# Optimization experiments

Measured on AMD Instinct MI355X. Metric: run time of the kernel, lower is better.

Reference implementation:

```python
import jax, jax.numpy as jnp
import numpy as np

V, E, H2, TAG = 32000, 128, 256, 9
H = H2 // 2          # per-direction LSTM hidden
B, T = 128, 512


def setup_inputs() -> dict:
    key = jax.random.key(0)
    ks = jax.random.split(key, 15)
    s = 0.08
    n = lambda k, shp: jax.random.normal(k, shp, dtype=jnp.float32) * s
    return {
        "sentence": jax.random.randint(ks[0], (B, T), 0, V, dtype=jnp.int32),
        "tags": jax.random.randint(ks[1], (B, T), 0, TAG, dtype=jnp.int32),
        "mask": jnp.ones((B, T), dtype=bool),
        "embedding": n(ks[2], (V, E)),
        "w_ih_f": n(ks[3], (4 * H, E)),
        "w_hh_f": n(ks[4], (4 * H, H)),
        "b_f": n(ks[5], (4 * H,)),
        "w_ih_b": n(ks[6], (4 * H, E)),
        "w_hh_b": n(ks[7], (4 * H, H)),
        "b_b": n(ks[8], (4 * H,)),
        "w_out": n(ks[9], (TAG, H2)),
        "b_out": n(ks[10], (TAG,)),
        "start_trans": n(ks[11], (TAG,)),
        "end_trans": n(ks[12], (TAG,)),
        "trans": n(ks[13], (TAG, TAG)),
    }


def _lstm_dir(xp, w_hh):
    """xp: [T,B,4H] precomputed input projections (incl. bias). Returns h seq [T,B,H]."""
    Hn = w_hh.shape[1]
    Bn = xp.shape[1]

    def step(carry, x_t):
        h, c = carry
        g = x_t + h @ w_hh.T                       # [B,4H]
        i, f, gg, o = jnp.split(g, 4, axis=-1)     # torch gate order: i,f,g,o
        c = jax.nn.sigmoid(f) * c + jax.nn.sigmoid(i) * jnp.tanh(gg)
        h = jax.nn.sigmoid(o) * jnp.tanh(c)
        return (h, c), h

    init = (jnp.zeros((Bn, Hn), xp.dtype), jnp.zeros((Bn, Hn), xp.dtype))
    _, hs = jax.lax.scan(step, init, xp)
    return hs


def reference(sentence, tags, mask, embedding, w_ih_f, w_hh_f, b_f,
              w_ih_b, w_hh_b, b_b, w_out, b_out, start_trans, end_trans, trans):
    # ---- BiLSTM emissions ----
    x = embedding[sentence]                 # [B,T,E]
    xt = jnp.swapaxes(x, 0, 1)              # [T,B,E]
    h_f = _lstm_dir(xt @ w_ih_f.T + b_f, w_hh_f)                 # [T,B,H]
    h_b = _lstm_dir((xt @ w_ih_b.T + b_b)[::-1], w_hh_b)[::-1]   # [T,B,H]
    hcat = jnp.concatenate([h_f, h_b], axis=-1)                  # [T,B,2H]
    emissions = hcat @ w_out.T + b_out                           # [T,B,TAG]

    m = mask.T.astype(emissions.dtype)      # [T,B]
    tt = tags.T                             # [T,B]
    bidx = jnp.arange(tt.shape[1])

    # ---- CRF numerator (score of gold path), torchcrf semantics ----
    num0 = start_trans[tt[0]] + emissions[0, bidx, tt[0]]        # [B]

    def num_step(score, inp):
        e_t, t_prev, t_cur, m_t = inp
        return score + (trans[t_prev, t_cur] + e_t[bidx, t_cur]) * m_t, None

    num, _ = jax.lax.scan(num_step, num0, (emissions[1:], tt[:-1], tt[1:], m[1:]))
    seq_ends = mask.sum(axis=1).astype(jnp.int32) - 1            # [B]
    last_tags = tt[seq_ends, bidx]
    num = num + end_trans[last_tags]

    # ---- CRF log-partition (forward algorithm) ----
    alpha0 = start_trans + emissions[0]                          # [B,TAG]

    def fwd_step(alpha, inp):
        e_t, m_t = inp
        nxt = jax.nn.logsumexp(alpha[:, :, None] + trans[None] + e_t[:, None, :], axis=1)
        return jnp.where(m_t[:, None] > 0, nxt, alpha), None

    alpha, _ = jax.lax.scan(fwd_step, alpha0, (emissions[1:], m[1:]))
    logZ = jax.nn.logsumexp(alpha + end_trans, axis=1)           # [B]

    # forward returns -crf(...) with reduction='mean' => mean negative log-likelihood
    return -jnp.mean(num - logZ)
```

## Files before the change

kernel.cpp:

```cpp
#include <hip/hip_runtime.h>
#include <hip/hip_bf16.h>
#include <cstdint>
#include <cstddef>

#define NB   128
#define NT   512
#define NE   128
#define NH   128
#define NG   512
#define NTAG 9

typedef __bf16 bf16;
typedef __bf16 bf16x4 __attribute__((ext_vector_type(4)));
typedef __bf16 bf16x8 __attribute__((ext_vector_type(8)));
typedef _Float16 f16;
typedef _Float16 f16x2 __attribute__((ext_vector_type(2)));
typedef _Float16 f16x8 __attribute__((ext_vector_type(8)));
typedef float  floatx4 __attribute__((ext_vector_type(4)));

__device__ __forceinline__ float bflo_f32(unsigned u) {
  union { unsigned x; float f; } c; c.x = u << 16; return c.f;
}
__device__ __forceinline__ float bfhi_f32(unsigned u) {
  union { unsigned x; float f; } c; c.x = u & 0xFFFF0000u; return c.f;
}
__device__ __forceinline__ f16x2 pkh(float a, float b) {
  return __builtin_bit_cast(f16x2, __builtin_amdgcn_cvt_pkrtz(a, b));
}
__device__ __forceinline__ void block_sync_lds() {
  asm volatile("s_waitcnt lgkmcnt(0)\n\ts_barrier" ::: "memory");
}

__device__ __forceinline__ f16x2 sigm_h(f16x2 x) {
  const f16x2 lo = {(f16)(-2.5f), (f16)(-2.5f)}, hi = {(f16)2.5f, (f16)2.5f};
  x = __builtin_elementwise_min(__builtin_elementwise_max(x, lo), hi);
  f16x2 t = x * x;
  f16x2 p = t * (f16)0.0010154f + (f16)(-0.019144f);
  p = t * p + (f16)0.24964f;
  return x * p + (f16)0.5f;
}
__device__ __forceinline__ f16x2 tanh_h(f16x2 x) {
  const f16x2 lo = {(f16)(-1.5f), (f16)(-1.5f)}, hi = {(f16)1.5f, (f16)1.5f};
  x = __builtin_elementwise_min(__builtin_elementwise_max(x, lo), hi);
  f16x2 t = x * x;
  f16x2 p = t * (f16)0.045172f + (f16)(-0.27334f);
  p = t * p + (f16)0.98976f;
  return x * p;
}

__global__ __launch_bounds__(256, 1) void k_prep(
    const float* __restrict__ emb, const float* __restrict__ w_ih_f,
    const float* __restrict__ w_ih_b, const int* __restrict__ sentence,
    bf16* __restrict__ embb, bf16* __restrict__ wihf, bf16* __restrict__ wihb,
    int* __restrict__ sentT)
{
  const int gid = blockIdx.x * 256 + threadIdx.x;
  const int gsz = gridDim.x * 256;
  for (int i = gid; i < 512000; i += gsz) {
    const float* s = emb + (size_t)i * 8;
    bf16x8 v;
    #pragma unroll
    for (int j = 0; j < 8; ++j) v[j] = (bf16)s[j];
    *(bf16x8*)&embb[(size_t)i * 8] = v;
  }
  for (int i = gid; i < 8192; i += gsz) {
    const float* s = w_ih_f + (size_t)i * 8;
    bf16x8 v;
    #pragma unroll
    for (int j = 0; j < 8; ++j) v[j] = (bf16)s[j];
    *(bf16x8*)&wihf[(size_t)i * 8] = v;
  }
  for (int i = gid; i < 8192; i += gsz) {
    const float* s = w_ih_b + (size_t)i * 8;
    bf16x8 v;
    #pragma unroll
    for (int j = 0; j < 8; ++j) v[j] = (bf16)s[j];
    *(bf16x8*)&wihb[(size_t)i * 8] = v;
  }
  for (int i = gid; i < NT * NB; i += gsz) {
    const int t = i >> 7, b = i & 127;
    sentT[i] = sentence[b * NT + t];
  }
}

__global__ __launch_bounds__(256, 1) void k_embed_proj(
    const int* __restrict__ sentT, const bf16* __restrict__ embb,
    const bf16* __restrict__ wihf, const bf16* __restrict__ wihb,
    const float* __restrict__ b_f, const float* __restrict__ b_b,
    bf16* __restrict__ xp_f, bf16* __restrict__ xp_b)
{
  __shared__ bf16 Cld[128 * 136];
  const int mb = blockIdx.x, nb = blockIdx.y;
  const int colbase = nb * 128;
  const int tid = threadIdx.x;
  const int wv = tid >> 6, lane = tid & 63;
  const int lrow = lane & 15, quad = lane >> 4;
  const int m0 = (wv & 1) * 64, n0 = (wv >> 1) * 64;

  int tokv[4];
  #pragma unroll
  for (int mt = 0; mt < 4; ++mt)
    tokv[mt] = sentT[mb * NB + m0 + mt * 16 + lrow];
  bf16x8 af[4][4];
  #pragma unroll
  for (int kk = 0; kk < 4; ++kk)
    #pragma unroll
    for (int mt = 0; mt < 4; ++mt)
      af[kk][mt] = *(const bf16x8*)&embb[(size_t)tokv[mt] * NE + kk * 32 + quad * 8];

  #pragma unroll
  for (int d = 0; d < 2; ++d) {
    const bf16* W     = (d == 0) ? (wihf + (size_t)nb * 128 * 128)
                                 : (wihb + (size_t)nb * 128 * 128);
    const float* bias = (d == 0) ? (b_f + colbase) : (b_b + colbase);
    bf16* outdir      = (d == 0) ? xp_f : xp_b;

    floatx4 acc[4][4] = {};
    #pragma unroll
    for (int kk = 0; kk < 4; ++kk) {
      bf16x8 bfr[4];
      #pragma unroll
      for (int nt = 0; nt < 4; ++nt)
        bfr[nt] = *(const bf16x8*)&W[(size_t)(n0 + nt * 16 + lrow) * 128 + kk * 32 + quad * 8];
      #pragma unroll
      for (int mt = 0; mt < 4; ++mt)
        #pragma unroll
        for (int nt = 0; nt < 4; ++nt)
          acc[mt][nt] = __builtin_amdgcn_mfma_f32_16x16x32_bf16(af[kk][mt], bfr[nt], acc[mt][nt], 0, 0, 0);
    }
    float bv[4];
    #pragma unroll
    for (int nt = 0; nt < 4; ++nt) bv[nt] = bias[n0 + nt * 16 + lrow];
    if (d == 1) __syncthreads();
    #pragma unroll
    for (int mt = 0; mt < 4; ++mt)
      #pragma unroll
      for (int nt = 0; nt < 4; ++nt) {
        bf16x4 v4;
        #pragma unroll
        for (int rr = 0; rr < 4; ++rr) v4[rr] = (bf16)(acc[mt][nt][rr] + bv[nt]);
        *(bf16x4*)&Cld[(n0 + nt * 16 + lrow) * 136 + m0 + mt * 16 + quad * 4] = v4;
      }
    __syncthreads();
    bf16* outbase = outdir + ((size_t)mb * 8) * (512 * 16) + (size_t)colbase * 16;
    #pragma unroll
    for (int it = 0; it < 8; ++it) {
      const int p = it * 256 + tid;
      const int bb = p >> 8, n = (p >> 1) & 127, half = p & 1;
      *(bf16x8*)(outbase + ((size_t)bb * 512 + n) * 16 + half * 8) =
          *(const bf16x8*)&Cld[n * 136 + bb * 16 + half * 8];
    }
  }
}

#define LSTM_STEP(PX, RB, WB)                                                  \
  do {                                                                         \
    f16x8 af[4];                                                               \
    _Pragma("unroll")                                                          \
    for (int kk = 0; kk < 4; ++kk)                                             \
      af[kk] = *(const f16x8*)&(RB)[lane * 8 + kk * 512];                      \
    floatx4 acc[4];                                                            \
    _Pragma("unroll")                                                          \
    for (int g = 0; g < 4; ++g) {                                              \
      acc[g][0] = bflo_f32(PX[g][0]); acc[g][1] = bfhi_f32(PX[g][0]);          \
      acc[g][2] = bflo_f32(PX[g][1]); acc[g][3] = bfhi_f32(PX[g][1]);          \
    }                                                                          \
    _Pragma("unroll")                                                          \
    for (int g = 0; g < 4; ++g) {             \
      uint2 u = *(const uint2*)pg[g];                                          \
      PX[g][0] = u.x; PX[g][1] = u.y;                                          \
      pg[g] += dstep_x;                                                        \
    }                                                                          \
    _Pragma("unroll")                                                          \
    for (int kk = 0; kk < 4; ++kk)                                             \
      _Pragma("unroll")                                                        \
      for (int g = 0; g < 4; ++g)                                              \
        acc[g] = __builtin_amdgcn_mfma_f32_16x16x32_f16(af[kk], wf[g][kk],     \
                                                        acc[g], 0, 0, 0);      \
    {                                                                          \
      f16x2 iv, fv, gv, ov, h2;                                                \
      iv = sigm_h(pkh(acc[0][0], acc[0][1]));                                  \
      fv = sigm_h(pkh(acc[1][0], acc[1][1]));                                  \
      gv = tanh_h(pkh(acc[2][0], acc[2][1]));                                  \
      ov = sigm_h(pkh(acc[3][0], acc[3][1]));                                  \
      c01 = fv * c01 + iv * gv;                                                \
      h2 = ov * tanh_h(c01);                                                   \
      (WB)[wboff + 0 * 8] = h2[0]; (WB)[wboff + 1 * 8] = h2[1];                \
      hop[0 * NH] = h2[0]; hop[1 * NH] = h2[1];                                \
      iv = sigm_h(pkh(acc[0][2], acc[0][3]));                                  \
      fv = sigm_h(pkh(acc[1][2], acc[1][3]));                                  \
      gv = tanh_h(pkh(acc[2][2], acc[2][3]));                                  \
      ov = sigm_h(pkh(acc[3][2], acc[3][3]));                                  \
      c23 = fv * c23 + iv * gv;                                                \
      h2 = ov * tanh_h(c23);                                                   \
      (WB)[wboff + 2 * 8] = h2[0]; (WB)[wboff + 3 * 8] = h2[1];                \
      hop[2 * NH] = h2[0]; hop[3 * NH] = h2[1];                                \
    }                                                                          \
    hop += dstep_h;                                                            \
    block_sync_lds();                                                          \
  } while (0)

__global__ __launch_bounds__(512, 1) void k_lstm(
    const bf16* __restrict__ xp_f, const bf16* __restrict__ xp_b,
    const float* __restrict__ w_hh_f, const float* __restrict__ w_hh_b,
    f16* __restrict__ h_f, f16* __restrict__ h_b)
{
  __shared__ f16 hfrag[2][2048];
  const int wg = blockIdx.x;
  const int dir = wg >> 3;
  const int bb = wg & 7;
  const int b0 = bb * 16;
  const bf16* __restrict__ xp   = dir ? xp_b   : xp_f;
  const float* __restrict__ Whh = dir ? w_hh_b : w_hh_f;
  f16* __restrict__ hout        = dir ? h_b    : h_f;
  const int tid = threadIdx.x;
  const int wv = tid >> 6, lane = tid & 63;
  const int lrow = lane & 15, quad = lane >> 4;
  const int hc = wv * 16 + lrow;

  f16x8 wf[4][4];
  #pragma unroll
  for (int g = 0; g < 4; ++g)
    #pragma unroll
    for (int kk = 0; kk < 4; ++kk) {
      const float* src = Whh + (size_t)(g * 128 + hc) * 128 + kk * 32 + quad * 8;
      f16x8 v;
      #pragma unroll
      for (int j = 0; j < 8; ++j) v[j] = (f16)src[j];
      wf[g][kk] = v;
    }
  {
    f16x2 z = {(f16)0.f, (f16)0.f};
    *(f16x2*)&hfrag[0][tid * 2] = z;
    *(f16x2*)&hfrag[0][1024 + tid * 2] = z;
  }

  const int t0 = dir ? (NT - 1) : 0;
  const ptrdiff_t dstep_x = dir ? -(ptrdiff_t)(8 * 512 * 16) : (ptrdiff_t)(8 * 512 * 16);
  const ptrdiff_t dstep_h = dir ? -(ptrdiff_t)(NB * NH) : (ptrdiff_t)(NB * NH);

  const bf16* pg[4];
  unsigned pxA[4][2], pxB[4][2];
  #pragma unroll
  for (int g = 0; g < 4; ++g)
    pg[g] = xp + (((size_t)t0 * 8 + bb) * 512 + g * 128 + hc) * 16 + quad * 4;
  #pragma unroll
  for (int g = 0; g < 4; ++g) {
    uint2 u = *(const uint2*)pg[g];
    pxA[g][0] = u.x; pxA[g][1] = u.y;
    pg[g] += dstep_x;
  }
  #pragma unroll
  for (int g = 0; g < 4; ++g) {
    uint2 u = *(const uint2*)pg[g];
    pxB[g][0] = u.x; pxB[g][1] = u.y;
    pg[g] += dstep_x;
  }
  f16* hop = hout + ((size_t)t0 * NB + b0 + quad * 4) * NH + hc;
  const int wboff = ((hc >> 3) * 16 + quad * 4) * 8 + (hc & 7);
  f16x2 c01 = {(f16)0.f, (f16)0.f}, c23 = {(f16)0.f, (f16)0.f};
  block_sync_lds();

  for (int s = 0; s < NT; s += 2) {
    LSTM_STEP(pxA, hfrag[0], hfrag[1]);
    LSTM_STEP(pxB, hfrag[1], hfrag[0]);
  }
}

__global__ __launch_bounds__(256, 1) void k_emis(
    const f16* __restrict__ h_f, const f16* __restrict__ h_b,
    const float* __restrict__ w_out, const float* __restrict__ b_out,
    float* __restrict__ emis)
{
  const int tid = threadIdx.x;
  const int wv = tid >> 6, lane = tid & 63;
  const int lrow = lane & 15, quad = lane >> 4;
  const int m0 = blockIdx.x * 64 + wv * 16;
  const size_t mrow = (size_t)(m0 + lrow);

  f16x8 wo[8];
  #pragma unroll
  for (int kk = 0; kk < 8; ++kk) {
    f16x8 v;
    #pragma unroll
    for (int j = 0; j < 8; ++j) v[j] = (f16)0.0f;
    if (lrow < NTAG) {
      const float* src = w_out + (size_t)lrow * 256 + kk * 32 + quad * 8;
      #pragma unroll
      for (int j = 0; j < 8; ++j) v[j] = (f16)src[j];
    }
    wo[kk] = v;
  }
  floatx4 acc = {};
  #pragma unroll
  for (int kk = 0; kk < 4; ++kk) {
    const f16x8 a = *(const f16x8*)&h_f[mrow * NH + kk * 32 + quad * 8];
    acc = __builtin_amdgcn_mfma_f32_16x16x32_f16(a, wo[kk], acc, 0, 0, 0);
  }
  #pragma unroll
  for (int kk = 0; kk < 4; ++kk) {
    const f16x8 a = *(const f16x8*)&h_b[mrow * NH + kk * 32 + quad * 8];
    acc = __builtin_amdgcn_mfma_f32_16x16x32_f16(a, wo[kk + 4], acc, 0, 0, 0);
  }
  if (lrow < NTAG) {
    const float bb = b_out[lrow];
    #pragma unroll
    for (int rr = 0; rr < 4; ++rr)
      emis[(size_t)(m0 + quad * 4 + rr) * NTAG + lrow] = acc[rr] + bb;
  }
}

__global__ __launch_bounds__(192, 1) void k_crfA(
    const float* __restrict__ emis, const float* __restrict__ trans,
    float* __restrict__ P)
{
  const int tid = threadIdx.x;
  const int grp = tid >> 4;
  const int j = tid & 15;
  const int c = blockIdx.x;
  const int b = blockIdx.y;
  const int gbase = (tid & 63) & ~15;
  const int i = (grp < 9) ? grp : 8;
  const int jj = (j < NTAG) ? j : 0;

  float tcol[NTAG];
  #pragma unroll
  for (int k = 0; k < NTAG; ++k) tcol[k] = trans[k * NTAG + jj];

  const int t1 = 1 + 8 * c;
  const int nst = (c == 63) ? 6 : 7;
  int eo = (t1 * NB + b) * NTAG + jj;
  float alpha = (j < NTAG) ? (trans[i * NTAG + jj] + emis[eo]) : -1e30f;
  for (int tt = 0; tt < nst; ++tt) {
    eo += NB * NTAG;
    const float e = emis[eo];
    float a[NTAG];
    #pragma unroll
    for (int k = 0; k < NTAG; ++k) a[k] = __shfl(alpha, gbase + k, 64) + tcol[k];
    float m = a[0];
    #pragma unroll
    for (int k = 1; k < NTAG; ++k) m = fmaxf(m, a[k]);
    float ssum = 0.0f;
    #pragma unroll
    for (int k = 0; k < NTAG; ++k) ssum += __expf(a[k] - m);
    alpha = m + __logf(ssum) + e;
  }
  if (grp < NTAG && j < NTAG)
    P[(((size_t)b * 64 + c) * NTAG + j) * NTAG + i] = alpha;
}

#define CHUNK_STEP(PC)                                                         \
  do {                                                                         \
    float a[NTAG];                                                             \
    _Pragma("unroll")                                                          \
    for (int k = 0; k < NTAG; ++k) a[k] = __shfl(alpha, gbase + k, 64) + PC[k];\
    float m = a[0];                                                            \
    _Pragma("unroll")                                                          \
    for (int k = 1; k < NTAG; ++k) m = fmaxf(m, a[k]);                         \
    float ssum = 0.0f;                                                         \
    _Pragma("unroll")                                                          \
    for (int k = 0; k < NTAG; ++k) ssum += __expf(a[k] - m);                   \
    alpha = m + __logf(ssum);                                                  \
  } while (0)

__global__ __launch_bounds__(256, 1) void k_crfB(
    const float* __restrict__ emis, const int* __restrict__ tags,
    const float* __restrict__ start_trans, const float* __restrict__ end_trans,
    const float* __restrict__ trans, const float* __restrict__ P,
    float* __restrict__ res)
{
  const int tid = threadIdx.x;
  const int grp = tid >> 4;
  const int j = tid & 15;
  const int b = blockIdx.x * 16 + grp;
  const int gbase = (tid & 63) & ~15;
  const int jj = (j < NTAG) ? j : 0;

  float nsum = 0.0f;
  for (int t = 1 + j; t < NT; t += 16) {
    const int tp = tags[b * NT + t - 1];
    const int tc = tags[b * NT + t];
    nsum += trans[tp * NTAG + tc] + emis[(t * NB + b) * NTAG + tc];
  }
  if (j == 0) {
    const int tg0 = tags[b * NT];
    const int tgl = tags[b * NT + NT - 1];
    nsum += start_trans[tg0] + emis[b * NTAG + tg0] + end_trans[tgl];
  }
  #pragma unroll
  for (int m = 8; m >= 1; m >>= 1) nsum += __shfl_xor(nsum, m, 16);

  float alpha = (j < NTAG) ? (start_trans[j] + emis[b * NTAG + jj]) : -1e30f;
  const float* Pb = P + ((size_t)b * 64 * 81) + jj * NTAG;
  float pA[NTAG], pB[NTAG];
  #pragma unroll
  for (int k = 0; k < NTAG; ++k) pA[k] = Pb[k];
  #pragma unroll
  for (int k = 0; k < NTAG; ++k) pB[k] = Pb[81 + k];
  for (int c = 0; c < 64; c += 2) {
    CHUNK_STEP(pA);
    if (c + 2 < 64) {
      #pragma unroll
      for (int k = 0; k < NTAG; ++k) pA[k] = Pb[(c + 2) * 81 + k];
    }
    CHUNK_STEP(pB);
    if (c + 3 < 64) {
      #pragma unroll
      for (int k = 0; k < NTAG; ++k) pB[k] = Pb[(c + 3) * 81 + k];
    }
  }
  const float av = (j < NTAG) ? (alpha + end_trans[j]) : -1e30f;
  float vals[NTAG];
  #pragma unroll
  for (int k = 0; k < NTAG; ++k) vals[k] = __shfl(av, gbase + k, 64);
  float m2 = vals[0];
  #pragma unroll
  for (int k = 1; k < NTAG; ++k) m2 = fmaxf(m2, vals[k]);
  float s2 = 0.0f;
  #pragma unroll
  for (int k = 0; k < NTAG; ++k) s2 += __expf(vals[k] - m2);
  const float logZ = m2 + __logf(s2);
  if (j == 0) res[b] = logZ - nsum;
}

__global__ __launch_bounds__(128, 1) void k_mean(const float* __restrict__ res,
                                                 float* __restrict__ out)
{
  const int tid = threadIdx.x;
  float v = res[tid];
  #pragma unroll
  for (int m = 32; m >= 1; m >>= 1) v += __shfl_xor(v, m, 64);
  __shared__ float sv[2];
  if ((tid & 63) == 0) sv[tid >> 6] = v;
  __syncthreads();
  if (tid == 0) out[0] = (sv[0] + sv[1]) * (1.0f / 128.0f);
}

extern "C" void kernel_launch(void* const* d_in, const int* in_sizes, int n_in,
                              void* d_out, int out_size, void* d_ws, size_t ws_size,
                              hipStream_t stream)
{
  (void)in_sizes; (void)n_in; (void)out_size; (void)ws_size;
  const int*   sentence    = (const int*)d_in[0];
  const int*   tags        = (const int*)d_in[1];
  const float* embedding   = (const float*)d_in[3];
  const float* w_ih_f      = (const float*)d_in[4];
  const float* w_hh_f      = (const float*)d_in[5];
  const float* b_f         = (const float*)d_in[6];
  const float* w_ih_b      = (const float*)d_in[7];
  const float* w_hh_b      = (const float*)d_in[8];
  const float* b_b         = (const float*)d_in[9];
  const float* w_out       = (const float*)d_in[10];
  const float* b_out       = (const float*)d_in[11];
  const float* start_trans = (const float*)d_in[12];
  const float* end_trans   = (const float*)d_in[13];
  const float* trans       = (const float*)d_in[14];
  float* out = (float*)d_out;

  char* ws = (char*)d_ws;
  bf16*  xp_f = (bf16*)(ws);
  bf16*  xp_b = (bf16*)(ws + 67108864);
  f16*   h_f  = (f16*)(ws + 134217728);
  f16*   h_b  = (f16*)(ws + 150994944);
  float* emis = (float*)(ws + 167772160);
  bf16*  embb  = (bf16*)(ws + 134217728);
  bf16*  wihf  = (bf16*)(ws + 142606336);
  bf16*  wihb  = (bf16*)(ws + 142737408);
  int*   sentT = (int*) (ws + 142868480);
  float* P     = (float*)(ws + 134217728);
  float* res   = (float*)(ws + 136871936);

  k_prep<<<256, 256, 0, stream>>>(embedding, w_ih_f, w_ih_b, sentence,
                                  embb, wihf, wihb, sentT);
  k_embed_proj<<<dim3(512, 4), 256, 0, stream>>>(sentT, embb, wihf, wihb,
                                                 b_f, b_b, xp_f, xp_b);
  k_lstm<<<16, 512, 0, stream>>>(xp_f, xp_b, w_hh_f, w_hh_b, h_f, h_b);
  k_emis<<<1024, 256, 0, stream>>>(h_f, h_b, w_out, b_out, emis);
  k_crfA<<<dim3(64, 128), 192, 0, stream>>>(emis, trans, P);
  k_crfB<<<8, 256, 0, stream>>>(emis, tags, start_trans, end_trans, trans, P, res);
  k_mean<<<1, 128, 0, stream>>>(res, out);
}
```

Before: 581.3 us.

## Halve LSTM workgroup to 4 waves, each handling two hidden-column slices

The recurrent LSTM kernel now runs 256 threads per block instead of 512, with each wave computing two 16-column hidden slices (cs=0,1) and holding twice the recurrent weight fragments in registers. This reduces the number of waves participating in the per-step block barrier and gives each wave more independent MFMA work to interleave. In exchange it doubles per-thread register use for weights and accumulators, which risks spills, and halves the available wave-level parallelism per step.

```diff
diff --git a/kernel.cpp b/kernel.cpp
--- a/kernel.cpp
+++ b/kernel.cpp
@@ -159,48 +159,60 @@
     _Pragma("unroll")                                                          \
     for (int kk = 0; kk < 4; ++kk)                                             \
       af[kk] = *(const f16x8*)&(RB)[lane * 8 + kk * 512];                      \
-    floatx4 acc[4];                                                            \
-    _Pragma("unroll")                                                          \
-    for (int g = 0; g < 4; ++g) {                                              \
-      acc[g][0] = bflo_f32(PX[g][0]); acc[g][1] = bfhi_f32(PX[g][0]);          \
-      acc[g][2] = bflo_f32(PX[g][1]); acc[g][3] = bfhi_f32(PX[g][1]);          \
-    }                                                                          \
-    _Pragma("unroll")                                                          \
-    for (int g = 0; g < 4; ++g) {             \
-      uint2 u = *(const uint2*)pg[g];                                          \
-      PX[g][0] = u.x; PX[g][1] = u.y;                                          \
-      pg[g] += dstep_x;                                                        \
-    }                                                                          \
+    floatx4 acc[2][4];                                                         \
+    _Pragma("unroll")                                                          \
+    for (int cs = 0; cs < 2; ++cs)                                             \
+      _Pragma("unroll")                                                        \
+      for (int g = 0; g < 4; ++g) {                                            \
+        acc[cs][g][0] = bflo_f32(PX[cs][g][0]);                                \
+        acc[cs][g][1] = bfhi_f32(PX[cs][g][0]);                                \
+        acc[cs][g][2] = bflo_f32(PX[cs][g][1]);                                \
+        acc[cs][g][3] = bfhi_f32(PX[cs][g][1]);                                \
+      }                                                                        \
+    _Pragma("unroll")                                                          \
+    for (int cs = 0; cs < 2; ++cs)            \
+      _Pragma("unroll")                                                        \
+      for (int g = 0; g < 4; ++g) {                                            \
+        uint2 u = *(const uint2*)(pg[g] + cs * 1024);                          \
+        PX[cs][g][0] = u.x; PX[cs][g][1] = u.y;                                \
+      }                                                                        \
+    _Pragma("unroll")                                                          \
+    for (int g = 0; g < 4; ++g) pg[g] += dstep_x;                              \
     _Pragma("unroll")                                                          \
     for (int kk = 0; kk < 4; ++kk)                                             \
       _Pragma("unroll")                                                        \
-      for (int g = 0; g < 4; ++g)                                              \
-        acc[g] = __builtin_amdgcn_mfma_f32_16x16x32_f16(af[kk], wf[g][kk],     \
-                                                        acc[g], 0, 0, 0);      \
-    {                                                                          \
+      for (int cs = 0; cs < 2; ++cs)                                           \
+        _Pragma("unroll")                                                      \
+        for (int g = 0; g < 4; ++g)                                            \
+          acc[cs][g] = __builtin_amdgcn_mfma_f32_16x16x32_f16(                 \
+              af[kk], wf[cs][g][kk], acc[cs][g], 0, 0, 0);                     \
+    _Pragma("unroll")                                                          \
+    for (int cs = 0; cs < 2; ++cs) {                                           \
       f16x2 iv, fv, gv, ov, h2;                                                \
-      iv = sigm_h(pkh(acc[0][0], acc[0][1]));                                  \
-      fv = sigm_h(pkh(acc[1][0], acc[1][1]));                                  \
-      gv = tanh_h(pkh(acc[2][0], acc[2][1]));                                  \
-      ov = sigm_h(pkh(acc[3][0], acc[3][1]));                                  \
-      c01 = fv * c01 + iv * gv;                                                \
-      h2 = ov * tanh_h(c01);                                                   \
-      (WB)[wboff + 0 * 8] = h2[0]; (WB)[wboff + 1 * 8] = h2[1];                \
-      hop[0 * NH] = h2[0]; hop[1 * NH] = h2[1];                                \
-      iv = sigm_h(pkh(acc[0][2], acc[0][3]));                                  \
-      fv = sigm_h(pkh(acc[1][2], acc[1][3]));                                  \
-      gv = tanh_h(pkh(acc[2][2], acc[2][3]));                                  \
-      ov = sigm_h(pkh(acc[3][2], acc[3][3]));                                  \
-      c23 = fv * c23 + iv * gv;                                                \
-      h2 = ov * tanh_h(c23);                                                   \
-      (WB)[wboff + 2 * 8] = h2[0]; (WB)[wboff + 3 * 8] = h2[1];                \
-      hop[2 * NH] = h2[0]; hop[3 * NH] = h2[1];                                \
+      iv = sigm_h(pkh(acc[cs][0][0], acc[cs][0][1]));                          \
+      fv = sigm_h(pkh(acc[cs][1][0], acc[cs][1][1]));                          \
+      gv = tanh_h(pkh(acc[cs][2][0], acc[cs][2][1]));                          \
+      ov = sigm_h(pkh(acc[cs][3][0], acc[cs][3][1]));                          \
+      c01[cs] = fv * c01[cs] + iv * gv;                                        \
+      h2 = ov * tanh_h(c01[cs]);                                               \
+      (WB)[wboff + cs * 1024 + 0 * 8] = h2[0];                                 \
+      (WB)[wboff + cs * 1024 + 1 * 8] = h2[1];                                 \
+      hop[cs * 64 + 0 * NH] = h2[0]; hop[cs * 64 + 1 * NH] = h2[1];            \
+      iv = sigm_h(pkh(acc[cs][0][2], acc[cs][0][3]));                          \
+      fv = sigm_h(pkh(acc[cs][1][2], acc[cs][1][3]));                          \
+      gv = tanh_h(pkh(acc[cs][2][2], acc[cs][2][3]));                          \
+      ov = sigm_h(pkh(acc[cs][3][2], acc[cs][3][3]));                          \
+      c23[cs] = fv * c23[cs] + iv * gv;                                        \
+      h2 = ov * tanh_h(c23[cs]);                                               \
+      (WB)[wboff + cs * 1024 + 2 * 8] = h2[0];                                 \
+      (WB)[wboff + cs * 1024 + 3 * 8] = h2[1];                                 \
+      hop[cs * 64 + 2 * NH] = h2[0]; hop[cs * 64 + 3 * NH] = h2[1];            \
     }                                                                          \
     hop += dstep_h;                                                            \
     block_sync_lds();                                                          \
   } while (0)
 
-__global__ __launch_bounds__(512, 1) void k_lstm(
+__global__ __launch_bounds__(256, 1) void k_lstm(
     const bf16* __restrict__ xp_f, const bf16* __restrict__ xp_b,
     const float* __restrict__ w_hh_f, const float* __restrict__ w_hh_b,
     f16* __restrict__ h_f, f16* __restrict__ h_b)
@@ -218,21 +230,24 @@
   const int lrow = lane & 15, quad = lane >> 4;
   const int hc = wv * 16 + lrow;
 
-  f16x8 wf[4][4];
-  #pragma unroll
-  for (int g = 0; g < 4; ++g)
-    #pragma unroll
-    for (int kk = 0; kk < 4; ++kk) {
-      const float* src = Whh + (size_t)(g * 128 + hc) * 128 + kk * 32 + quad * 8;
-      f16x8 v;
-      #pragma unroll
-      for (int j = 0; j < 8; ++j) v[j] = (f16)src[j];
-      wf[g][kk] = v;
-    }
+  f16x8 wf[2][4][4];
+  #pragma unroll
+  for (int cs = 0; cs < 2; ++cs)
+    #pragma unroll
+    for (int g = 0; g < 4; ++g)
+      #pragma unroll
+      for (int kk = 0; kk < 4; ++kk) {
+        const float* src = Whh + (size_t)(g * 128 + cs * 64 + hc) * 128 + kk * 32 + quad * 8;
+        f16x8 v;
+        #pragma unroll
+        for (int j = 0; j < 8; ++j) v[j] = (f16)src[j];
+        wf[cs][g][kk] = v;
+      }
   {
-    f16x2 z = {(f16)0.f, (f16)0.f};
-    *(f16x2*)&hfrag[0][tid * 2] = z;
-    *(f16x2*)&hfrag[0][1024 + tid * 2] = z;
+    f16x8 z;
+    #pragma unroll
+    for (int j = 0; j < 8; ++j) z[j] = (f16)0.f;
+    *(f16x8*)&hfrag[0][tid * 8] = z;
   }
 
   const int t0 = dir ? (NT - 1) : 0;
@@ -240,25 +255,37 @@
   const ptrdiff_t dstep_h = dir ? -(ptrdiff_t)(NB * NH) : (ptrdiff_t)(NB * NH);
 
   const bf16* pg[4];
-  unsigned pxA[4][2], pxB[4][2];
+  unsigned pxA[2][4][2], pxB[2][4][2];
   #pragma unroll
   for (int g = 0; g < 4; ++g)
     pg[g] = xp + (((size_t)t0 * 8 + bb) * 512 + g * 128 + hc) * 16 + quad * 4;
   #pragma unroll
-  for (int g = 0; g < 4; ++g) {
-    uint2 u = *(const uint2*)pg[g];
-    pxA[g][0] = u.x; pxA[g][1] = u.y;
-    pg[g] += dstep_x;
-  }
-  #pragma unroll
-  for (int g = 0; g < 4; ++g) {
-    uint2 u = *(const uint2*)pg[g];
-    pxB[g][0] = u.x; pxB[g][1] = u.y;
-    pg[g] += dstep_x;
-  }
+  for (int cs = 0; cs < 2; ++cs)
+    #pragma unroll
+    for (int g = 0; g < 4; ++g) {
+      uint2 u = *(const uint2*)(pg[g] + cs * 1024);
+      pxA[cs][g][0] = u.x; pxA[cs][g][1] = u.y;
+    }
+  #pragma unroll
+  for (int g = 0; g < 4; ++g) pg[g] += dstep_x;
+  #pragma unroll
+  for (int cs = 0; cs < 2; ++cs)
+    #pragma unroll
+    for (int g = 0; g < 4; ++g) {
+      uint2 u = *(const uint2*)(pg[g] + cs * 1024);
+      pxB[cs][g][0] = u.x; pxB[cs][g][1] = u.y;
+    }
+  #pragma unroll
+  for (int g = 0; g < 4; ++g) pg[g] += dstep_x;
+
   f16* hop = hout + ((size_t)t0 * NB + b0 + quad * 4) * NH + hc;
   const int wboff = ((hc >> 3) * 16 + quad * 4) * 8 + (hc & 7);
-  f16x2 c01 = {(f16)0.f, (f16)0.f}, c23 = {(f16)0.f, (f16)0.f};
+  f16x2 c01[2], c23[2];
+  #pragma unroll
+  for (int cs = 0; cs < 2; ++cs) {
+    c01[cs][0] = (f16)0.f; c01[cs][1] = (f16)0.f;
+    c23[cs][0] = (f16)0.f; c23[cs][1] = (f16)0.f;
+  }
   block_sync_lds();
 
   for (int s = 0; s < NT; s += 2) {
@@ -474,7 +501,7 @@
                                   embb, wihf, wihb, sentT);
   k_embed_proj<<<dim3(512, 4), 256, 0, stream>>>(sentT, embb, wihf, wihb,
                                                  b_f, b_b, xp_f, xp_b);
-  k_lstm<<<16, 512, 0, stream>>>(xp_f, xp_b, w_hh_f, w_hh_b, h_f, h_b);
+  k_lstm<<<16, 256, 0, stream>>>(xp_f, xp_b, w_hh_f, w_hh_b, h_f, h_b);
   k_emis<<<1024, 256, 0, stream>>>(h_f, h_b, w_out, b_out, emis);
   k_crfA<<<dim3(64, 128), 192, 0, stream>>>(emis, trans, P);
   k_crfB<<<8, 256, 0, stream>>>(emis, tags, start_trans, end_trans, trans, P, res);
```

Result: slower. 746.3 us (+28.4%).

## Fuse CRF combine and mean reduction into chunk kernel via atomic counters

Applied to the files above, without the earlier changes.

The CRF chunk kernel now counts finished chunks per batch element with an atomic counter. The last block for each batch element then runs the gold-path score and the chunk-combine log-partition, and a global counter lets the final block compute the mean. The counters are zeroed in the emission kernel. This removes two kernel launches and their gaps, at the cost of atomics, fences and a serialized tail in a few blocks.

```diff
diff --git a/kernel.cpp b/kernel.cpp
--- a/kernel.cpp
+++ b/kernel.cpp
@@ -270,9 +270,13 @@
 __global__ __launch_bounds__(256, 1) void k_emis(
     const f16* __restrict__ h_f, const f16* __restrict__ h_b,
     const float* __restrict__ w_out, const float* __restrict__ b_out,
-    float* __restrict__ emis)
+    float* __restrict__ emis, int* __restrict__ cnt_b, int* __restrict__ cnt_all)
 {
   const int tid = threadIdx.x;
+  if (blockIdx.x == 0) {
+    if (tid < 128) cnt_b[tid] = 0;
+    if (tid == 128) *cnt_all = 0;
+  }
   const int wv = tid >> 6, lane = tid & 63;
   const int lrow = lane & 15, quad = lane >> 4;
   const int m0 = blockIdx.x * 64 + wv * 16;
@@ -310,10 +314,29 @@
   }
 }
 
+#define CHUNK_STEP(PC)                                                         \
+  do {                                                                         \
+    float a[NTAG];                                                             \
+    _Pragma("unroll")                                                          \
+    for (int k = 0; k < NTAG; ++k) a[k] = __shfl(alpha, gbase + k, 64) + PC[k];\
+    float m = a[0];                                                            \
+    _Pragma("unroll")                                                          \
+    for (int k = 1; k < NTAG; ++k) m = fmaxf(m, a[k]);                         \
+    float ssum = 0.0f;                                                         \
+    _Pragma("unroll")                                                          \
+    for (int k = 0; k < NTAG; ++k) ssum += __expf(a[k] - m);                   \
+    alpha = m + __logf(ssum);                                                  \
+  } while (0)
+
 __global__ __launch_bounds__(192, 1) void k_crfA(
     const float* __restrict__ emis, const float* __restrict__ trans,
-    float* __restrict__ P)
-{
+    const int* __restrict__ tags, const float* __restrict__ start_trans,
+    const float* __restrict__ end_trans, float* __restrict__ P,
+    int* __restrict__ cnt_b, int* __restrict__ cnt_all,
+    float* __restrict__ res, float* __restrict__ out)
+{
+  __shared__ int s_last;
+  __shared__ float sv[2];
   const int tid = threadIdx.x;
   const int grp = tid >> 4;
   const int j = tid & 15;
@@ -323,115 +346,108 @@
   const int i = (grp < 9) ? grp : 8;
   const int jj = (j < NTAG) ? j : 0;
 
-  float tcol[NTAG];
-  #pragma unroll
-  for (int k = 0; k < NTAG; ++k) tcol[k] = trans[k * NTAG + jj];
-
-  const int t1 = 1 + 8 * c;
-  const int nst = (c == 63) ? 6 : 7;
-  int eo = (t1 * NB + b) * NTAG + jj;
-  float alpha = (j < NTAG) ? (trans[i * NTAG + jj] + emis[eo]) : -1e30f;
-  for (int tt = 0; tt < nst; ++tt) {
-    eo += NB * NTAG;
-    const float e = emis[eo];
-    float a[NTAG];
-    #pragma unroll
-    for (int k = 0; k < NTAG; ++k) a[k] = __shfl(alpha, gbase + k, 64) + tcol[k];
-    float m = a[0];
-    #pragma unroll
-    for (int k = 1; k < NTAG; ++k) m = fmaxf(m, a[k]);
-    float ssum = 0.0f;
-    #pragma unroll
-    for (int k = 0; k < NTAG; ++k) ssum += __expf(a[k] - m);
-    alpha = m + __logf(ssum) + e;
-  }
-  if (grp < NTAG && j < NTAG)
-    P[(((size_t)b * 64 + c) * NTAG + j) * NTAG + i] = alpha;
-}
-
-#define CHUNK_STEP(PC)                                                         \
-  do {                                                                         \
-    float a[NTAG];                                                             \
-    _Pragma("unroll")                                                          \
-    for (int k = 0; k < NTAG; ++k) a[k] = __shfl(alpha, gbase + k, 64) + PC[k];\
-    float m = a[0];                                                            \
-    _Pragma("unroll")                                                          \
-    for (int k = 1; k < NTAG; ++k) m = fmaxf(m, a[k]);                         \
-    float ssum = 0.0f;                                                         \
-    _Pragma("unroll")                                                          \
-    for (int k = 0; k < NTAG; ++k) ssum += __expf(a[k] - m);                   \
-    alpha = m + __logf(ssum);                                                  \
-  } while (0)
-
-__global__ __launch_bounds__(256, 1) void k_crfB(
-    const float* __restrict__ emis, const int* __restrict__ tags,
-    const float* __restrict__ start_trans, const float* __restrict__ end_trans,
-    const float* __restrict__ trans, const float* __restrict__ P,
-    float* __restrict__ res)
-{
-  const int tid = threadIdx.x;
-  const int grp = tid >> 4;
-  const int j = tid & 15;
-  const int b = blockIdx.x * 16 + grp;
-  const int gbase = (tid & 63) & ~15;
-  const int jj = (j < NTAG) ? j : 0;
-
-  float nsum = 0.0f;
-  for (int t = 1 + j; t < NT; t += 16) {
-    const int tp = tags[b * NT + t - 1];
-    const int tc = tags[b * NT + t];
-    nsum += trans[tp * NTAG + tc] + emis[(t * NB + b) * NTAG + tc];
-  }
-  if (j == 0) {
-    const int tg0 = tags[b * NT];
-    const int tgl = tags[b * NT + NT - 1];
-    nsum += start_trans[tg0] + emis[b * NTAG + tg0] + end_trans[tgl];
-  }
-  #pragma unroll
-  for (int m = 8; m >= 1; m >>= 1) nsum += __shfl_xor(nsum, m, 16);
-
-  float alpha = (j < NTAG) ? (start_trans[j] + emis[b * NTAG + jj]) : -1e30f;
-  const float* Pb = P + ((size_t)b * 64 * 81) + jj * NTAG;
-  float pA[NTAG], pB[NTAG];
-  #pragma unroll
-  for (int k = 0; k < NTAG; ++k) pA[k] = Pb[k];
-  #pragma unroll
-  for (int k = 0; k < NTAG; ++k) pB[k] = Pb[81 + k];
-  for (int c = 0; c < 64; c += 2) {
-    CHUNK_STEP(pA);
-    if (c + 2 < 64) {
-      #pragma unroll
-      for (int k = 0; k < NTAG; ++k) pA[k] = Pb[(c + 2) * 81 + k];
-    }
-    CHUNK_STEP(pB);
-    if (c + 3 < 64) {
-      #pragma unroll
-      for (int k = 0; k < NTAG; ++k) pB[k] = Pb[(c + 3) * 81 + k];
-    }
-  }
-  const float av = (j < NTAG) ? (alpha + end_trans[j]) : -1e30f;
-  float vals[NTAG];
-  #pragma unroll
-  for (int k = 0; k < NTAG; ++k) vals[k] = __shfl(av, gbase + k, 64);
-  float m2 = vals[0];
-  #pragma unroll
-  for (int k = 1; k < NTAG; ++k) m2 = fmaxf(m2, vals[k]);
-  float s2 = 0.0f;
-  #pragma unroll
-  for (int k = 0; k < NTAG; ++k) s2 += __expf(vals[k] - m2);
-  const float logZ = m2 + __logf(s2);
-  if (j == 0) res[b] = logZ - nsum;
-}
-
-__global__ __launch_bounds__(128, 1) void k_mean(const float* __restrict__ res,
-                                                 float* __restrict__ out)
-{
-  const int tid = threadIdx.x;
-  float v = res[tid];
-  #pragma unroll
-  for (int m = 32; m >= 1; m >>= 1) v += __shfl_xor(v, m, 64);
-  __shared__ float sv[2];
-  if ((tid & 63) == 0) sv[tid >> 6] = v;
+  {
+    float tcol[NTAG];
+    #pragma unroll
+    for (int k = 0; k < NTAG; ++k) tcol[k] = trans[k * NTAG + jj];
+
+    const int t1 = 1 + 8 * c;
+    const int nst = (c == 63) ? 6 : 7;
+    int eo = (t1 * NB + b) * NTAG + jj;
+    float alpha = (j < NTAG) ? (trans[i * NTAG + jj] + emis[eo]) : -1e30f;
+    for (int tt = 0; tt < nst; ++tt) {
+      eo += NB * NTAG;
+      const float e = emis[eo];
+      float a[NTAG];
+      #pragma unroll
+      for (int k = 0; k < NTAG; ++k) a[k] = __shfl(alpha, gbase + k, 64) + tcol[k];
+      float m = a[0];
+      #pragma unroll
+      for (int k = 1; k < NTAG; ++k) m = fmaxf(m, a[k]);
+      float ssum = 0.0f;
+      #pragma unroll
+      for (int k = 0; k < NTAG; ++k) ssum += __expf(a[k] - m);
+      alpha = m + __logf(ssum) + e;
+    }
+    if (grp < NTAG && j < NTAG)
+      P[(((size_t)b * 64 + c) * NTAG + j) * NTAG + i] = alpha;
+  }
+
+  __syncthreads();
+  if (tid == 0) {
+    __threadfence();
+    s_last = (atomicAdd(&cnt_b[b], 1) == 63) ? 1 : 0;
+  }
+  __syncthreads();
+  if (!s_last) return;
+  __threadfence();
+
+  {
+    float nsum = 0.0f;
+    if (tid < 16) {
+      for (int t = 1 + tid; t < NT; t += 16) {
+        const int tp = tags[b * NT + t - 1];
+        const int tc = tags[b * NT + t];
+        nsum += trans[tp * NTAG + tc] + emis[(t * NB + b) * NTAG + tc];
+      }
+      if (tid == 0) {
+        const int tg0 = tags[b * NT];
+        const int tgl = tags[b * NT + NT - 1];
+        nsum += start_trans[tg0] + emis[b * NTAG + tg0] + end_trans[tgl];
+      }
+      #pragma unroll
+      for (int m = 8; m >= 1; m >>= 1) nsum += __shfl_xor(nsum, m, 16);
+
+      const int j2 = (tid < NTAG) ? tid : 0;
+      float alpha = (tid < NTAG) ? (start_trans[tid] + emis[b * NTAG + j2]) : -1e30f;
+      const float* Pb = P + ((size_t)b * 64 * 81) + j2 * NTAG;
+      float pA[NTAG], pB[NTAG];
+      #pragma unroll
+      for (int k = 0; k < NTAG; ++k) pA[k] = Pb[k];
+      #pragma unroll
+      for (int k = 0; k < NTAG; ++k) pB[k] = Pb[81 + k];
+      for (int cc = 0; cc < 64; cc += 2) {
+        CHUNK_STEP(pA);
+        if (cc + 2 < 64) {
+          #pragma unroll
+          for (int k = 0; k < NTAG; ++k) pA[k] = Pb[(cc + 2) * 81 + k];
+        }
+        CHUNK_STEP(pB);
+        if (cc + 3 < 64) {
+          #pragma unroll
+          for (int k = 0; k < NTAG; ++k) pB[k] = Pb[(cc + 3) * 81 + k];
+        }
+      }
+      const float av = (tid < NTAG) ? (alpha + end_trans[tid]) : -1e30f;
+      float vals[NTAG];
+      #pragma unroll
+      for (int k = 0; k < NTAG; ++k) vals[k] = __shfl(av, k, 64);
+      float m2 = vals[0];
+      #pragma unroll
+      for (int k = 1; k < NTAG; ++k) m2 = fmaxf(m2, vals[k]);
+      float s2 = 0.0f;
+      #pragma unroll
+      for (int k = 0; k < NTAG; ++k) s2 += __expf(vals[k] - m2);
+      const float logZ = m2 + __logf(s2);
+      if (tid == 0) res[b] = logZ - nsum;
+    }
+  }
+
+  __threadfence();
+  __syncthreads();
+  if (tid == 0) {
+    s_last = (atomicAdd(cnt_all, 1) == 127) ? 1 : 0;
+  }
+  __syncthreads();
+  if (!s_last) return;
+  __threadfence();
+
+  if (tid < 128) {
+    float v = res[tid];
+    #pragma unroll
+    for (int m = 32; m >= 1; m >>= 1) v += __shfl_xor(v, m, 64);
+    if ((tid & 63) == 0) sv[tid >> 6] = v;
+  }
   __syncthreads();
   if (tid == 0) out[0] = (sv[0] + sv[1]) * (1.0f / 128.0f);
 }
@@ -469,14 +485,15 @@
   int*   sentT = (int*) (ws + 142868480);
   float* P     = (float*)(ws + 134217728);
   float* res   = (float*)(ws + 136871936);
+  int*   cnt_b   = (int*)(ws);
+  int*   cnt_all = (int*)(ws + 512);
 
   k_prep<<<256, 256, 0, stream>>>(embedding, w_ih_f, w_ih_b, sentence,
                                   embb, wihf, wihb, sentT);
   k_embed_proj<<<dim3(512, 4), 256, 0, stream>>>(sentT, embb, wihf, wihb,
                                                  b_f, b_b, xp_f, xp_b);
   k_lstm<<<16, 512, 0, stream>>>(xp_f, xp_b, w_hh_f, w_hh_b, h_f, h_b);
-  k_emis<<<1024, 256, 0, stream>>>(h_f, h_b, w_out, b_out, emis);
-  k_crfA<<<dim3(64, 128), 192, 0, stream>>>(emis, trans, P);
-  k_crfB<<<8, 256, 0, stream>>>(emis, tags, start_trans, end_trans, trans, P, res);
-  k_mean<<<1, 128, 0, stream>>>(res, out);
-}
+  k_emis<<<1024, 256, 0, stream>>>(h_f, h_b, w_out, b_out, emis, cnt_b, cnt_all);
+  k_crfA<<<dim3(64, 128), 192, 0, stream>>>(emis, trans, tags, start_trans,
+                                            end_trans, P, cnt_b, cnt_all, res, out);
+}
```

Result: slower. 801.0 us (+37.8%).

## Fuse CRF chunk and combine kernels into one per-batch block using LDS

Applied to the files above, without the earlier changes.

Merges the two CRF kernels into a single kernel with one 1024-thread block per sequence. The block computes the 64x9 chunk transfer matrices into shared memory instead of global memory, computes the gold-path numerator in parallel with 512 threads, then has 16 threads run the sequential chunk combine. This removes a kernel launch and the global round-trip of P, and spreads the numerator across many threads. The trade-offs are that only 128 blocks are launched and the chunk work now runs in 9 serial rounds per block.

```diff
diff --git a/kernel.cpp b/kernel.cpp
--- a/kernel.cpp
+++ b/kernel.cpp
@@ -310,117 +310,102 @@
   }
 }
 
-__global__ __launch_bounds__(192, 1) void k_crfA(
+__global__ __launch_bounds__(1024, 1) void k_crf(
     const float* __restrict__ emis, const float* __restrict__ trans,
-    float* __restrict__ P)
-{
+    const int* __restrict__ tags, const float* __restrict__ start_trans,
+    const float* __restrict__ end_trans, float* __restrict__ res)
+{
+  __shared__ float Pl[64 * 81];
+  __shared__ float nred[8];
+  const int b = blockIdx.x;
   const int tid = threadIdx.x;
   const int grp = tid >> 4;
   const int j = tid & 15;
-  const int c = blockIdx.x;
-  const int b = blockIdx.y;
-  const int gbase = (tid & 63) & ~15;
-  const int i = (grp < 9) ? grp : 8;
-  const int jj = (j < NTAG) ? j : 0;
-
-  float tcol[NTAG];
-  #pragma unroll
-  for (int k = 0; k < NTAG; ++k) tcol[k] = trans[k * NTAG + jj];
-
-  const int t1 = 1 + 8 * c;
-  const int nst = (c == 63) ? 6 : 7;
-  int eo = (t1 * NB + b) * NTAG + jj;
-  float alpha = (j < NTAG) ? (trans[i * NTAG + jj] + emis[eo]) : -1e30f;
-  for (int tt = 0; tt < nst; ++tt) {
-    eo += NB * NTAG;
-    const float e = emis[eo];
-    float a[NTAG];
-    #pragma unroll
-    for (int k = 0; k < NTAG; ++k) a[k] = __shfl(alpha, gbase + k, 64) + tcol[k];
-    float m = a[0];
-    #pragma unroll
-    for (int k = 1; k < NTAG; ++k) m = fmaxf(m, a[k]);
-    float ssum = 0.0f;
-    #pragma unroll
-    for (int k = 0; k < NTAG; ++k) ssum += __expf(a[k] - m);
-    alpha = m + __logf(ssum) + e;
-  }
-  if (grp < NTAG && j < NTAG)
-    P[(((size_t)b * 64 + c) * NTAG + j) * NTAG + i] = alpha;
-}
-
-#define CHUNK_STEP(PC)                                                         \
-  do {                                                                         \
-    float a[NTAG];                                                             \
-    _Pragma("unroll")                                                          \
-    for (int k = 0; k < NTAG; ++k) a[k] = __shfl(alpha, gbase + k, 64) + PC[k];\
-    float m = a[0];                                                            \
-    _Pragma("unroll")                                                          \
-    for (int k = 1; k < NTAG; ++k) m = fmaxf(m, a[k]);                         \
-    float ssum = 0.0f;                                                         \
-    _Pragma("unroll")                                                          \
-    for (int k = 0; k < NTAG; ++k) ssum += __expf(a[k] - m);                   \
-    alpha = m + __logf(ssum);                                                  \
-  } while (0)
-
-__global__ __launch_bounds__(256, 1) void k_crfB(
-    const float* __restrict__ emis, const int* __restrict__ tags,
-    const float* __restrict__ start_trans, const float* __restrict__ end_trans,
-    const float* __restrict__ trans, const float* __restrict__ P,
-    float* __restrict__ res)
-{
-  const int tid = threadIdx.x;
-  const int grp = tid >> 4;
-  const int j = tid & 15;
-  const int b = blockIdx.x * 16 + grp;
   const int gbase = (tid & 63) & ~15;
   const int jj = (j < NTAG) ? j : 0;
 
-  float nsum = 0.0f;
-  for (int t = 1 + j; t < NT; t += 16) {
-    const int tp = tags[b * NT + t - 1];
-    const int tc = tags[b * NT + t];
-    nsum += trans[tp * NTAG + tc] + emis[(t * NB + b) * NTAG + tc];
-  }
-  if (j == 0) {
-    const int tg0 = tags[b * NT];
-    const int tgl = tags[b * NT + NT - 1];
-    nsum += start_trans[tg0] + emis[b * NTAG + tg0] + end_trans[tgl];
-  }
-  #pragma unroll
-  for (int m = 8; m >= 1; m >>= 1) nsum += __shfl_xor(nsum, m, 16);
-
-  float alpha = (j < NTAG) ? (start_trans[j] + emis[b * NTAG + jj]) : -1e30f;
-  const float* Pb = P + ((size_t)b * 64 * 81) + jj * NTAG;
-  float pA[NTAG], pB[NTAG];
-  #pragma unroll
-  for (int k = 0; k < NTAG; ++k) pA[k] = Pb[k];
-  #pragma unroll
-  for (int k = 0; k < NTAG; ++k) pB[k] = Pb[81 + k];
-  for (int c = 0; c < 64; c += 2) {
-    CHUNK_STEP(pA);
-    if (c + 2 < 64) {
-      #pragma unroll
-      for (int k = 0; k < NTAG; ++k) pA[k] = Pb[(c + 2) * 81 + k];
-    }
-    CHUNK_STEP(pB);
-    if (c + 3 < 64) {
-      #pragma unroll
-      for (int k = 0; k < NTAG; ++k) pB[k] = Pb[(c + 3) * 81 + k];
-    }
-  }
-  const float av = (j < NTAG) ? (alpha + end_trans[j]) : -1e30f;
-  float vals[NTAG];
-  #pragma unroll
-  for (int k = 0; k < NTAG; ++k) vals[k] = __shfl(av, gbase + k, 64);
-  float m2 = vals[0];
-  #pragma unroll
-  for (int k = 1; k < NTAG; ++k) m2 = fmaxf(m2, vals[k]);
-  float s2 = 0.0f;
-  #pragma unroll
-  for (int k = 0; k < NTAG; ++k) s2 += __expf(vals[k] - m2);
-  const float logZ = m2 + __logf(s2);
-  if (j == 0) res[b] = logZ - nsum;
+  float tcol[NTAG];
+  #pragma unroll
+  for (int k = 0; k < NTAG; ++k) tcol[k] = trans[k * NTAG + jj];
+
+  for (int round = 0; round < 9; ++round) {
+    const int task = round * 64 + grp;
+    const int c = task / 9;
+    const int i = task - c * 9;
+    const int t1 = 1 + 8 * c;
+    const int nst = (c == 63) ? 6 : 7;
+    int eo = (t1 * NB + b) * NTAG + jj;
+    float alpha = (j < NTAG) ? (trans[i * NTAG + jj] + emis[eo]) : -1e30f;
+    for (int tt = 0; tt < 7; ++tt) {
+      if (tt < nst) {
+        eo += NB * NTAG;
+        const float e = emis[eo];
+        float a[NTAG];
+        #pragma unroll
+        for (int k = 0; k < NTAG; ++k) a[k] = __shfl(alpha, gbase + k, 64) + tcol[k];
+        float m = a[0];
+        #pragma unroll
+        for (int k = 1; k < NTAG; ++k) m = fmaxf(m, a[k]);
+        float ssum = 0.0f;
+        #pragma unroll
+        for (int k = 0; k < NTAG; ++k) ssum += __expf(a[k] - m);
+        alpha = m + __logf(ssum) + e;
+      }
+    }
+    if (j < NTAG) Pl[c * 81 + j * 9 + i] = alpha;
+  }
+
+  if (tid >= 512) {
+    const int k = tid - 512;
+    float nval;
+    if (k == 0) {
+      const int tg0 = tags[b * NT];
+      const int tgl = tags[b * NT + NT - 1];
+      nval = start_trans[tg0] + emis[b * NTAG + tg0] + end_trans[tgl];
+    } else {
+      const int tp = tags[b * NT + k - 1];
+      const int tc = tags[b * NT + k];
+      nval = trans[tp * NTAG + tc] + emis[(k * NB + b) * NTAG + tc];
+    }
+    #pragma unroll
+    for (int m = 32; m >= 1; m >>= 1) nval += __shfl_xor(nval, m, 64);
+    if ((tid & 63) == 0) nred[(tid >> 6) - 8] = nval;
+  }
+  __syncthreads();
+
+  if (tid < 16) {
+    float alpha = (tid < NTAG) ? (start_trans[tid] + emis[b * NTAG + jj]) : -1e30f;
+    for (int c = 0; c < 64; ++c) {
+      const float* Pc = &Pl[c * 81 + jj * 9];
+      float a[NTAG];
+      #pragma unroll
+      for (int k = 0; k < NTAG; ++k) a[k] = __shfl(alpha, k, 64) + Pc[k];
+      float m = a[0];
+      #pragma unroll
+      for (int k = 1; k < NTAG; ++k) m = fmaxf(m, a[k]);
+      float ssum = 0.0f;
+      #pragma unroll
+      for (int k = 0; k < NTAG; ++k) ssum += __expf(a[k] - m);
+      alpha = m + __logf(ssum);
+    }
+    const float av = (tid < NTAG) ? (alpha + end_trans[tid]) : -1e30f;
+    float vals[NTAG];
+    #pragma unroll
+    for (int k = 0; k < NTAG; ++k) vals[k] = __shfl(av, k, 64);
+    float m2 = vals[0];
+    #pragma unroll
+    for (int k = 1; k < NTAG; ++k) m2 = fmaxf(m2, vals[k]);
+    float s2 = 0.0f;
+    #pragma unroll
+    for (int k = 0; k < NTAG; ++k) s2 += __expf(vals[k] - m2);
+    const float logZ = m2 + __logf(s2);
+    if (tid == 0) {
+      float nsum = 0.0f;
+      #pragma unroll
+      for (int w = 0; w < 8; ++w) nsum += nred[w];
+      res[b] = logZ - nsum;
+    }
+  }
 }
 
 __global__ __launch_bounds__(128, 1) void k_mean(const float* __restrict__ res,
@@ -467,7 +452,6 @@
   bf16*  wihf  = (bf16*)(ws + 142606336);
   bf16*  wihb  = (bf16*)(ws + 142737408);
   int*   sentT = (int*) (ws + 142868480);
-  float* P     = (float*)(ws + 134217728);
   float* res   = (float*)(ws + 136871936);
 
   k_prep<<<256, 256, 0, stream>>>(embedding, w_ih_f, w_ih_b, sentence,
@@ -476,7 +460,6 @@
                                                  b_f, b_b, xp_f, xp_b);
   k_lstm<<<16, 512, 0, stream>>>(xp_f, xp_b, w_hh_f, w_hh_b, h_f, h_b);
   k_emis<<<1024, 256, 0, stream>>>(h_f, h_b, w_out, b_out, emis);
-  k_crfA<<<dim3(64, 128), 192, 0, stream>>>(emis, trans, P);
-  k_crfB<<<8, 256, 0, stream>>>(emis, tags, start_trans, end_trans, trans, P, res);
+  k_crf<<<128, 1024, 0, stream>>>(emis, trans, tags, start_trans, end_trans, res);
   k_mean<<<1, 128, 0, stream>>>(res, out);
 }
```

New measurement: 563.8 us. 1.03x faster.
